# Optimization experiments

Hardware: AMD Instinct MI355X
Metric: run time of the kernel (lower is better)

The kernel has to match this reference:

```python
import jax, jax.numpy as jnp
import numpy as np
import math

B, S, E, H, NL, OUT, VOCAB = 16, 512, 1024, 16, 6, 10, 16
D = E // H
PAD = VOCAB - 1
EPS = 1e-5


def _positional_encoding():
    # Faithful to the module: pe[:x.size(0)] indexes the BATCH dim of a
    # [B, S, E] tensor, yielding [B, 1, E] broadcast over sequence.
    pos = jnp.arange(B, dtype=jnp.float32)[:, None]            # [B,1]
    div = jnp.exp(jnp.arange(0, E, 2, dtype=jnp.float32) * (-math.log(10000.0) / E))
    pe = jnp.zeros((B, E), dtype=jnp.float32)
    pe = pe.at[:, 0::2].set(jnp.sin(pos * div))
    pe = pe.at[:, 1::2].set(jnp.cos(pos * div))
    return pe[:, None, :]                                      # [B,1,E]


def setup_inputs() -> dict:
    key = jax.random.key(0)
    ks = jax.random.split(key, 8)
    sc = 0.02
    return {
        "inputs": jax.random.randint(ks[0], (B, S), 0, PAD),   # no pad tokens
        "emb": jax.random.normal(ks[1], (VOCAB, E), jnp.float32) * sc,
        "wq": jax.random.normal(ks[2], (E, E), jnp.float32) * sc,
        "bq": jnp.zeros((E,), jnp.float32),
        "wk": jax.random.normal(ks[3], (E, E), jnp.float32) * sc,
        "bk": jnp.zeros((E,), jnp.float32),
        "wv": jax.random.normal(ks[4], (E, E), jnp.float32) * sc,
        "bv": jnp.zeros((E,), jnp.float32),
        "wfc": jax.random.normal(ks[5], (E, E), jnp.float32) * sc,
        "bfc": jnp.zeros((E,), jnp.float32),
        "gamma": jnp.ones((E,), jnp.float32),
        "beta": jnp.zeros((E,), jnp.float32),
        "wout": jax.random.normal(ks[6], (S * E, OUT), jnp.float32) * sc,
        "bout": jnp.zeros((OUT,), jnp.float32),
    }


def _layernorm(x, gamma, beta):
    mu = jnp.mean(x, axis=-1, keepdims=True)
    var = jnp.mean(jnp.square(x - mu), axis=-1, keepdims=True)
    return (x - mu) * jax.lax.rsqrt(var + EPS) * gamma + beta


def reference(inputs, emb, wq, bq, wk, bk, wv, bv, wfc, bfc, gamma, beta, wout, bout):
    x = emb[inputs]                                            # [B,S,E]
    x = x + (x + _positional_encoding())                       # x += pos_enc(x)
    mask = (inputs == PAD)                                     # [B,S] key-pad mask
    scale = 1.0 / math.sqrt(D)
    for _ in range(NL):  # same (shared) weights each iteration, as in source
        q = (x @ wq + bq).reshape(B, S, H, D).transpose(0, 2, 1, 3)
        k = (x @ wk + bk).reshape(B, S, H, D).transpose(0, 2, 1, 3)
        v = (x @ wv + bv).reshape(B, S, H, D).transpose(0, 2, 1, 3)
        att = jnp.einsum('bhqd,bhkd->bhqk', q, k) * scale      # [B,H,S,S]
        att = jnp.where(mask[:, None, None, :], -jnp.inf, att)
        att = jax.nn.softmax(att, axis=-1)
        o = jnp.einsum('bhqk,bhkd->bhqd', att, v)
        o = o.transpose(0, 2, 1, 3).reshape(B, S, E)
        x = _layernorm(o + x, gamma, beta)                     # dropout = eval identity
        x = _layernorm((x @ wfc + bfc) + x, gamma, beta)
    return x.reshape(B, -1) @ wout + bout                      # [B,OUT]
```

## Files before the change

kernel.cpp:

```cpp
#include <hip/hip_runtime.h>
#include <hip/hip_bf16.h>
#include <math.h>

#define B_   16
#define S_   512
#define E_   1024
#define H_   16
#define D_   64
#define NL_  6
#define OUT_ 10
#define M_   (B_*S_)

typedef short short8 __attribute__((ext_vector_type(8)));
typedef float f32x4 __attribute__((ext_vector_type(4)));
typedef int   int4v __attribute__((ext_vector_type(4)));
typedef unsigned short ushort4v __attribute__((ext_vector_type(4)));

typedef const __attribute__((address_space(1))) unsigned int* gas1_t;
typedef __attribute__((address_space(3))) unsigned int* las3_t;
#define GLD16(g,l) __builtin_amdgcn_global_load_lds((gas1_t)(g), (las3_t)(l), 16, 0, 0)

static __device__ __forceinline__ float bf2f(unsigned short u){
  union { unsigned int i; float f; } v; v.i = ((unsigned int)u) << 16; return v.f;
}
static __device__ __forceinline__ unsigned short f2bf(float f){
  union { float f; unsigned int i; } v; v.f = f;
  unsigned int r = v.i + 0x7fffu + ((v.i >> 16) & 1u);
  return (unsigned short)(r >> 16);
}
static __device__ __forceinline__ f32x4 mfma16(short8 a, short8 b, f32x4 c){
  return __builtin_amdgcn_mfma_f32_16x16x32_bf16(a, b, c, 0, 0, 0);
}

__global__ __launch_bounds__(192)
void code_k(float* __restrict__ out, float code)
{
  int t = threadIdx.x;
  if (t < B_*OUT_) out[t] = code;
}

__global__ __launch_bounds__(256)
void transpose_k(const float* __restrict__ w0, const float* __restrict__ w1,
                 const float* __restrict__ w2, const float* __restrict__ w3,
                 unsigned short* __restrict__ wT)
{
  const float* w = blockIdx.z==0 ? w0 : blockIdx.z==1 ? w1 : blockIdx.z==2 ? w2 : w3;
  unsigned short* o = wT + (size_t)blockIdx.z * E_ * E_;
  __shared__ unsigned short tl[64][65];
  int n0 = blockIdx.x*64, k0 = blockIdx.y*64;
  int tx = threadIdx.x, ty = threadIdx.y;
  #pragma unroll
  for (int i = 0; i < 16; ++i)
    tl[ty + 4*i][tx] = f2bf(w[(size_t)(k0 + ty + 4*i)*E_ + n0 + tx]);
  __syncthreads();
  #pragma unroll
  for (int i = 0; i < 16; ++i)
    o[(size_t)(n0 + ty + 4*i)*E_ + k0 + tx] = tl[tx][ty + 4*i];
}

__global__ __launch_bounds__(256)
void embed_k(const int* __restrict__ tok, const float* __restrict__ emb,
             float* __restrict__ x, unsigned short* __restrict__ xb)
{
  int row = blockIdx.x;
  int b = row >> 9;
  int tk = tok[row];
  tk = tk < 0 ? 0 : (tk > 15 ? 15 : tk);
  int e0 = threadIdx.x * 4;
  const float c0 = -9.210340371976184f / (float)E_;
  f32x4 ev = *(const f32x4*)&emb[(size_t)tk * E_ + e0];
  f32x4 vv; ushort4v bb;
  #pragma unroll
  for (int i = 0; i < 4; ++i) {
    int e = e0 + i;
    float dv = expf((float)(e & ~1) * c0);
    float arg = (float)b * dv;
    float pe = (e & 1) ? cosf(arg) : sinf(arg);
    float v = 2.0f * ev[i] + pe;
    vv[i] = v; bb[i] = f2bf(v);
  }
  *(f32x4*)&x[(size_t)row*E_ + e0] = vv;
  *(ushort4v*)&xb[(size_t)row*E_ + e0] = bb;
}

template<int MODE>
__global__ __launch_bounds__(256)
void gemm_bt_k(const unsigned short* __restrict__ A,
               const unsigned short* __restrict__ BT,
               const float* __restrict__ biasA, const float* __restrict__ biasB,
               unsigned short* __restrict__ outq)
{
  __shared__ alignas(16) unsigned short SM[(MODE==2) ? 17408 : 16384];
  unsigned short* Al = SM;
  unsigned short* Bl = SM + 8192;
  int mt = blockIdx.x;
  int nyt = blockIdx.y;
  int wsel = (MODE == 0) ? (nyt >> 3) : 0;
  int nt   = (MODE == 0) ? (nyt & 7) : nyt;
  const unsigned short* Bp = BT + (size_t)wsel * E_ * E_ + (size_t)nt * 128 * E_;
  const float* bias = (MODE == 0) ? (wsel == 0 ? biasA : biasB) : biasA;
  int tid = threadIdx.x;
  int lane = tid & 63, wid = tid >> 6;
  int wr = wid >> 1, wc = wid & 1;
  int m0 = mt * 128;
  int lr = lane & 15, lk = lane >> 4;
  int lx = lr & 7;
  int c8 = tid & 7;
  int rbase = tid >> 3;
  int c8s = c8 ^ (rbase & 7);
  f32x4 acc[4][4] = {};
  for (int kt = 0; kt < E_/64; ++kt) {
    #pragma unroll
    for (int j = 0; j < 4; ++j) {
      int r = j*32 + rbase;
      int idx = j*256 + tid;
      GLD16(A + (size_t)(m0 + r)*E_ + kt*64 + c8s*8, &Al[idx*8]);
      GLD16(Bp + (size_t)r*E_ + kt*64 + c8s*8, &Bl[idx*8]);
    }
    __syncthreads();
    #pragma unroll
    for (int kk = 0; kk < 2; ++kk) {
      int sA = ((kk*4 + lk) ^ lx) * 8;
      short8 af[4], bfr[4];
      #pragma unroll
      for (int mi = 0; mi < 4; ++mi)
        af[mi] = *(const short8*)&Al[(wr*64 + mi*16 + lr)*64 + sA];
      #pragma unroll
      for (int ni = 0; ni < 4; ++ni)
        bfr[ni] = *(const short8*)&Bl[(wc*64 + ni*16 + lr)*64 + sA];
      #pragma unroll
      for (int mi = 0; mi < 4; ++mi)
        #pragma unroll
        for (int ni = 0; ni < 4; ++ni)
          acc[mi][ni] = mfma16(af[mi], bfr[ni], acc[mi][ni]);
    }
    __syncthreads();
  }
  if (MODE == 2) {
    unsigned short* Ct = SM;
    #pragma unroll
    for (int ni = 0; ni < 4; ++ni) {
      int nl = wc*64 + ni*16 + lr;
      float bv = bias[nt*128 + nl];
      #pragma unroll
      for (int mi = 0; mi < 4; ++mi)
        #pragma unroll
        for (int j = 0; j < 4; ++j)
          Ct[nl*136 + wr*64 + mi*16 + lk*4 + j] = f2bf(acc[mi][ni][j] + bv);
    }
    __syncthreads();
    int dl = tid >> 1, half = tid & 1;
    int h = nt*2 + (dl >> 6), d = dl & 63;
    int bb = m0 >> 9, s0 = (m0 & 511) + half*64;
    unsigned short* gp = outq + (((size_t)(bb*H_ + h)*D_ + d)*S_ + s0);
    #pragma unroll
    for (int c = 0; c < 8; ++c)
      *(int4v*)(gp + c*8) = *(const int4v*)&Ct[dl*136 + half*64 + c*8];
  } else {
    unsigned short* Cl = SM;
    #pragma unroll
    for (int ni = 0; ni < 4; ++ni) {
      int n = nt*128 + wc*64 + ni*16 + lr;
      float bv = bias[n];
      #pragma unroll
      for (int mi = 0; mi < 4; ++mi)
        #pragma unroll
        for (int j = 0; j < 4; ++j)
          Cl[(wr*64 + mi*16 + lk*4 + j)*128 + wc*64 + ni*16 + lr] =
            f2bf(acc[mi][ni][j] + bv);
    }
    __syncthreads();
    int r = tid >> 1, half = tid & 1;
    int m = m0 + r;
    unsigned short* gp;
    if (MODE == 0) {
      int bb = m >> 9, s = m & 511;
      int h = nt*2 + half;
      gp = outq + (size_t)wsel*M_*E_ + (((size_t)(bb*H_ + h)*S_ + s)*D_);
    } else {
      gp = outq + (size_t)m*E_ + nt*128 + half*64;
    }
    const unsigned short* sp = &Cl[r*128 + half*64];
    #pragma unroll
    for (int c = 0; c < 8; ++c)
      *(int4v*)(gp + c*8) = *(const int4v*)(sp + c*8);
  }
}

__global__ __launch_bounds__(512, 4)
void attn_k(const unsigned short* __restrict__ Q, const unsigned short* __restrict__ K,
            const unsigned short* __restrict__ VT, unsigned short* __restrict__ O)
{
  extern __shared__ unsigned short SMEM[];
  int bid = blockIdx.x;
  int bh = bid & 255, qh = bid >> 8;
  int tid = threadIdx.x, lane = tid & 63, wid = tid >> 6;
  int lr = lane & 15, lk = lane >> 4;
  const unsigned short* Qb = Q + (size_t)bh * S_ * D_;
  const unsigned short* Kb = K + (size_t)bh * S_ * D_;
  const unsigned short* VTb = VT + (size_t)bh * S_ * D_;
  unsigned short* Pw = SMEM + 32768 + wid * 640;

  int kr  = tid >> 3, kc8 = tid & 7;
  int kcs = kc8 ^ (kr & 7);
  int vd  = tid >> 4, vc16 = tid & 15;
  int vcs = vc16 ^ (vd & 15);

  short8 qf[2][2];
  #pragma unroll
  for (int s = 0; s < 2; ++s) {
    int q0 = (qh*2 + s)*128 + wid*16;
    qf[s][0] = *(const short8*)(Qb + (size_t)(q0 + lr)*D_ + lk*8);
    qf[s][1] = *(const short8*)(Qb + (size_t)(q0 + lr)*D_ + 32 + lk*8);
  }

  {
    unsigned short* Kd = SMEM;
    unsigned short* Vd = SMEM + 16384;
    #pragma unroll
    for (int j = 0; j < 2; ++j) {
      int idx = j*512 + tid;
      int r = (j*512 + tid) >> 3;
      (void)r;
      GLD16(Kb + (size_t)(kr + j*64)*D_ + kcs*8, &Kd[idx*8]);
      GLD16(VTb + (size_t)(vd)*S_ + (j*64 + 0)*0 + 0 + ((size_t)0) + (vcs*8) + ((size_t)(j)*0), &Vd[idx*8]);
    }
  }
  __syncthreads();

  {
    unsigned short* Vd = SMEM + 16384;
    #pragma unroll
    for (int j = 0; j < 2; ++j) {
      int idx = j*512 + tid;
      int d = idx >> 4, c16 = idx & 15;
      int cs = c16 ^ (d & 15);
      GLD16(VTb + (size_t)d*S_ + cs*8, &Vd[idx*8]);
    }
  }
  __syncthreads();

  f32x4 oacc[2][4] = {};
  float plsum[2][4] = {{0.f,0.f,0.f,0.f},{0.f,0.f,0.f,0.f}};
  int cur = 0;
  for (int kt = 0; kt < 4; ++kt) {
    if (kt < 3) {
      unsigned short* Kd = SMEM + (cur^1)*8192;
      unsigned short* Vd = SMEM + 16384 + (cur^1)*8192;
      #pragma unroll
      for (int j = 0; j < 2; ++j) {
        int idx = j*512 + tid;
        int r = idx >> 3, c8 = idx & 7;
        GLD16(Kb + (size_t)((kt+1)*128 + r)*D_ + (c8 ^ (r & 7))*8, &Kd[idx*8]);
        int d = idx >> 4, c16 = idx & 15;
        GLD16(VTb + (size_t)d*S_ + (kt+1)*128 + (c16 ^ (d & 15))*8, &Vd[idx*8]);
      }
    }
    const unsigned short* Kl = SMEM + cur*8192;
    const unsigned short* Vl = SMEM + 16384 + cur*8192;
    #pragma unroll
    for (int s = 0; s < 2; ++s) {
      #pragma unroll
      for (int c = 0; c < 4; ++c) {
        f32x4 s0 = {}, s1 = {};
        {
          const unsigned short* kr0 = &Kl[((2*c)*16 + lr)*64];
          const unsigned short* kr1 = &Kl[((2*c+1)*16 + lr)*64];
          int a0 = ((lk     ^ (lr & 7)))*8;
          int a1 = (((4+lk) ^ (lr & 7)))*8;
          s0 = mfma16(qf[s][0], *(const short8*)(kr0 + a0), s0);
          s0 = mfma16(qf[s][1], *(const short8*)(kr0 + a1), s0);
          s1 = mfma16(qf[s][0], *(const short8*)(kr1 + a0), s1);
          s1 = mfma16(qf[s][1], *(const short8*)(kr1 + a1), s1);
        }
        #pragma unroll
        for (int j = 0; j < 4; ++j) {
          s0[j] = __expf(s0[j] * 0.125f);
          s1[j] = __expf(s1[j] * 0.125f);
          plsum[s][j] += s0[j] + s1[j];
        }
        #pragma unroll
        for (int j = 0; j < 4; ++j) {
          Pw[(lk*4 + j)*40 + lr]      = f2bf(s0[j]);
          Pw[(lk*4 + j)*40 + 16 + lr] = f2bf(s1[j]);
        }
        asm volatile("s_waitcnt lgkmcnt(0)" ::: "memory");
        short8 pf = *(const short8*)&Pw[lr*40 + lk*8];
        #pragma unroll
        for (int dt = 0; dt < 4; ++dt) {
          int drow = dt*16 + lr;
          short8 vf = *(const short8*)&Vl[drow*128 + (((c*4 + lk) ^ lr))*8];
          oacc[s][dt] = mfma16(pf, vf, oacc[s][dt]);
        }
      }
    }
    __syncthreads();
    cur ^= 1;
  }
  #pragma unroll
  for (int s = 0; s < 2; ++s) {
    float lsum[4];
    #pragma unroll
    for (int j = 0; j < 4; ++j) {
      float t = plsum[s][j];
      #pragma unroll
      for (int m = 1; m < 16; m <<= 1) t += __shfl_xor(t, m);
      lsum[j] = t;
    }
    int q0 = (qh*2 + s)*128 + wid*16;
    #pragma unroll
    for (int dt = 0; dt < 4; ++dt)
      #pragma unroll
      for (int j = 0; j < 4; ++j)
        O[(size_t)bh*S_*D_ + (size_t)(q0 + lk*4 + j)*D_ + dt*16 + lr] =
          f2bf(oacc[s][dt][j] / lsum[j]);
  }
}

template<bool PERM>
__global__ __launch_bounds__(256)
void ln_k(const unsigned short* __restrict__ g, float* __restrict__ x,
          unsigned short* __restrict__ xb,
          const float* __restrict__ gamma, const float* __restrict__ beta)
{
  int row = blockIdx.x;
  int tid = threadIdx.x;
  int e0 = tid * 4;
  ushort4v gu;
  if (PERM) {
    int b = row >> 9, s = row & 511;
    int h = e0 >> 6, d = e0 & 63;
    gu = *(const ushort4v*)&g[(((size_t)(b*H_ + h)*S_) + s)*D_ + d];
  } else {
    gu = *(const ushort4v*)&g[(size_t)row*E_ + e0];
  }
  f32x4 xv = *(const f32x4*)&x[(size_t)row*E_ + e0];
  f32x4 v;
  #pragma unroll
  for (int i = 0; i < 4; ++i) v[i] = bf2f(gu[i]) + xv[i];
  float sum = v[0]+v[1]+v[2]+v[3];
  float sq  = v[0]*v[0]+v[1]*v[1]+v[2]*v[2]+v[3]*v[3];
  #pragma unroll
  for (int m = 1; m < 64; m <<= 1) { sum += __shfl_xor(sum, m); sq += __shfl_xor(sq, m); }
  __shared__ float red[2][4];
  int lane = tid & 63, wid = tid >> 6;
  if (lane == 0) { red[0][wid] = sum; red[1][wid] = sq; }
  __syncthreads();
  float ts = red[0][0]+red[0][1]+red[0][2]+red[0][3];
  float tq = red[1][0]+red[1][1]+red[1][2]+red[1][3];
  float mu = ts * (1.0f/E_);
  float var = tq * (1.0f/E_) - mu*mu;
  float rsq = rsqrtf(var + 1e-5f);
  f32x4 y; ushort4v yb;
  #pragma unroll
  for (int i = 0; i < 4; ++i) {
    float t = (v[i]-mu)*rsq*gamma[e0+i] + beta[e0+i];
    y[i] = t; yb[i] = f2bf(t);
  }
  *(f32x4*)&x[(size_t)row*E_ + e0] = y;
  *(ushort4v*)&xb[(size_t)row*E_ + e0] = yb;
}

__global__ __launch_bounds__(256)
void outp_k(const float* __restrict__ x, const float* __restrict__ wout,
            float* __restrict__ part)
{
  int b = blockIdx.y;
  int chunk = blockIdx.x;
  int tid = threadIdx.x;
  float acc[OUT_] = {};
  const float* xr = x + (size_t)b * S_ * E_;
  for (int j = 0; j < 32; ++j) {
    int k = chunk*8192 + j*256 + tid;
    float xv = xr[k];
    const float* wr = wout + (size_t)k * OUT_;
    #pragma unroll
    for (int o = 0; o < OUT_; ++o) acc[o] += xv * wr[o];
  }
  #pragma unroll
  for (int o = 0; o < OUT_; ++o)
    #pragma unroll
    for (int m = 1; m < 64; m <<= 1) acc[o] += __shfl_xor(acc[o], m);
  __shared__ float red[4][OUT_];
  int lane = tid & 63, wid = tid >> 6;
  if (lane == 0) {
    #pragma unroll
    for (int o = 0; o < OUT_; ++o) red[wid][o] = acc[o];
  }
  __syncthreads();
  if (tid < OUT_) {
    float s = red[0][tid] + red[1][tid] + red[2][tid] + red[3][tid];
    part[((size_t)chunk*B_ + b)*OUT_ + tid] = s;
  }
}

__global__ __launch_bounds__(192)
void outred_k(const float* __restrict__ part, const float* __restrict__ bout,
              float* __restrict__ out)
{
  int t = threadIdx.x;
  if (t < B_*OUT_) {
    int b = t / OUT_, o = t % OUT_;
    float s = 0.f;
    for (int c = 0; c < 64; ++c) s += part[((size_t)c*B_ + b)*OUT_ + o];
    s += bout[o];
    out[t] = s;
  }
}

extern "C" void kernel_launch(void* const* d_in, const int* in_sizes, int n_in,
                              void* d_out, int out_size, void* d_ws, size_t ws_size,
                              hipStream_t stream)
{
  (void)out_size;
  float* outb = (float*)d_out;

  static const int expect[14] = {8192, 16384, 1048576, 1024, 1048576, 1024,
                                 1048576, 1024, 1048576, 1024, 1024, 1024,
                                 5242880, 10};
  if (n_in != 14) { code_k<<<dim3(1), dim3(192), 0, stream>>>(outb, 9000.0f); return; }
  for (int i = 0; i < 14; ++i)
    if (in_sizes[i] != expect[i]) {
      code_k<<<dim3(1), dim3(192), 0, stream>>>(outb, 5000.0f + 100.0f*i); return;
    }

  const int* tok = (const int*)d_in[0];
  const float* emb  = (const float*)d_in[1];
  const float* wq   = (const float*)d_in[2];
  const float* bq   = (const float*)d_in[3];
  const float* wk   = (const float*)d_in[4];
  const float* bk   = (const float*)d_in[5];
  const float* wv   = (const float*)d_in[6];
  const float* bv   = (const float*)d_in[7];
  const float* wfc  = (const float*)d_in[8];
  const float* bfc  = (const float*)d_in[9];
  const float* gam  = (const float*)d_in[10];
  const float* bet  = (const float*)d_in[11];
  const float* wout = (const float*)d_in[12];
  const float* bout = (const float*)d_in[13];

  char* ws = (char*)d_ws;
  size_t off = 0;
  unsigned short* wT = (unsigned short*)(ws + off); off += (size_t)4*E_*E_*2;
  float* x  = (float*)(ws + off);                   off += (size_t)M_*E_*4;
  unsigned short* xb = (unsigned short*)(ws + off); off += (size_t)M_*E_*2;
  unsigned short* qkvb = (unsigned short*)(ws + off); off += (size_t)3*M_*E_*2;
  unsigned short* gb = (unsigned short*)(ws + off); off += (size_t)M_*E_*2;
  float* part = (float*)(ws + off);                 off += (size_t)64*B_*OUT_*4;
  if (off > ws_size) { code_k<<<dim3(1), dim3(192), 0, stream>>>(outb, 9500.0f); return; }

  transpose_k<<<dim3(16,16,4), dim3(64,4), 0, stream>>>(wq, wk, wv, wfc, wT);
  embed_k<<<dim3(M_), dim3(256), 0, stream>>>(tok, emb, x, xb);
  unsigned short* qb = qkvb;
  unsigned short* kb = qkvb + (size_t)M_*E_;
  unsigned short* vb = qkvb + (size_t)2*M_*E_;
  for (int l = 0; l < NL_; ++l) {
    gemm_bt_k<0><<<dim3(64,16), dim3(256), 0, stream>>>(xb, wT, bq, bk, qkvb);
    gemm_bt_k<2><<<dim3(64,8),  dim3(256), 0, stream>>>(xb, wT + (size_t)2*E_*E_, bv, bv, vb);
    attn_k<<<dim3(512), dim3(512), 75776, stream>>>(qb, kb, vb, gb);
    ln_k<true><<<dim3(M_), dim3(256), 0, stream>>>(gb, x, xb, gam, bet);
    gemm_bt_k<1><<<dim3(64,8), dim3(256), 0, stream>>>(xb, wT + (size_t)3*E_*E_, bfc, bfc, gb);
    ln_k<false><<<dim3(M_), dim3(256), 0, stream>>>(gb, x, xb, gam, bet);
  }
  outp_k<<<dim3(64,B_), dim3(256), 0, stream>>>(x, wout, part);
  outred_k<<<dim3(1), dim3(192), 0, stream>>>(part, bout, outb);
}
```

Before: 1.040 ms.

## Replace 128x128 GEMMs with double-buffered 256x256 GEMM and fuse QKV launches

Introduces a 512-thread GEMM kernel with 256x256 output tiles and double-buffered LDS. It issues global_load_lds prefetches for the next k-tile in four phases, each followed by explicit vmcnt waits and barriers, and raises wave priority around the MFMA section. Q, K and V projections now run in a single launch, with V transposed through LDS in the epilogue, while Q/K and the FC output use direct scattered bf16 stores. The attention kernel also drops a redundant initial V tile load and one barrier. The larger tiles cut redundant operand loads, but the grids shrink to 384 and 128 blocks with 128KB of LDS each, which risks idle CUs and wave imbalance, especially for the FC projection.

New measurement: 1.075 ms. 1.03x slower.

```diff
diff --git a/kernel.cpp b/kernel.cpp
--- a/kernel.cpp
+++ b/kernel.cpp
@@ -19,6 +19,7 @@
 typedef const __attribute__((address_space(1))) unsigned int* gas1_t;
 typedef __attribute__((address_space(3))) unsigned int* las3_t;
 #define GLD16(g,l) __builtin_amdgcn_global_load_lds((gas1_t)(g), (las3_t)(l), 16, 0, 0)
+#define VMW(n) asm volatile("s_waitcnt vmcnt(" #n ")" ::: "memory")
 
 static __device__ __forceinline__ float bf2f(unsigned short u){
   union { unsigned int i; float f; } v; v.i = ((unsigned int)u) << 16; return v.f;
@@ -84,106 +85,143 @@
 }
 
 template<int MODE>
-__global__ __launch_bounds__(256)
-void gemm_bt_k(const unsigned short* __restrict__ A,
-               const unsigned short* __restrict__ BT,
-               const float* __restrict__ biasA, const float* __restrict__ biasB,
-               unsigned short* __restrict__ outq)
-{
-  __shared__ alignas(16) unsigned short SM[(MODE==2) ? 17408 : 16384];
-  unsigned short* Al = SM;
-  unsigned short* Bl = SM + 8192;
-  int mt = blockIdx.x;
-  int nyt = blockIdx.y;
-  int wsel = (MODE == 0) ? (nyt >> 3) : 0;
-  int nt   = (MODE == 0) ? (nyt & 7) : nyt;
-  const unsigned short* Bp = BT + (size_t)wsel * E_ * E_ + (size_t)nt * 128 * E_;
-  const float* bias = (MODE == 0) ? (wsel == 0 ? biasA : biasB) : biasA;
-  int tid = threadIdx.x;
-  int lane = tid & 63, wid = tid >> 6;
-  int wr = wid >> 1, wc = wid & 1;
-  int m0 = mt * 128;
-  int lr = lane & 15, lk = lane >> 4;
-  int lx = lr & 7;
-  int c8 = tid & 7;
-  int rbase = tid >> 3;
-  int c8s = c8 ^ (rbase & 7);
-  f32x4 acc[4][4] = {};
-  for (int kt = 0; kt < E_/64; ++kt) {
-    #pragma unroll
-    for (int j = 0; j < 4; ++j) {
-      int r = j*32 + rbase;
-      int idx = j*256 + tid;
-      GLD16(A + (size_t)(m0 + r)*E_ + kt*64 + c8s*8, &Al[idx*8]);
-      GLD16(Bp + (size_t)r*E_ + kt*64 + c8s*8, &Bl[idx*8]);
+__global__ __launch_bounds__(512, 2)
+void gemm256_k(const unsigned short* __restrict__ A,
+               const unsigned short* __restrict__ WT,
+               const float* __restrict__ bq, const float* __restrict__ bk,
+               const float* __restrict__ bv,
+               unsigned short* __restrict__ out)
+{
+  extern __shared__ unsigned short SM2[];
+  int mt = blockIdx.x, nt = blockIdx.y;
+  int wsel = (MODE==0) ? (nt>>2) : 3;
+  int ntl  = (MODE==0) ? (nt&3)  : nt;
+  const unsigned short* Bp = WT + (MODE==0 ? (size_t)wsel*E_*E_ : (size_t)0) + (size_t)ntl*256*E_;
+  const float* bias = (MODE==0) ? (wsel==0 ? bq : (wsel==1 ? bk : bv)) : bq;
+  int m0 = mt*256;
+  int tid = threadIdx.x, lane = tid&63, wid = tid>>6;
+  int lr = lane&15, lk = lane>>4;
+  int rl = tid>>3;
+  int cs = (tid&7) ^ (rl&7);
+  unsigned short* Ab0 = SM2;
+  unsigned short* Ab1 = SM2 + 16384;
+  unsigned short* Bb0 = SM2 + 32768;
+  unsigned short* Bb1 = SM2 + 49152;
+
+  f32x4 acc[16][2] = {};
+
+  auto stA = [&](unsigned short* dst, int kt, int q) {
+    GLD16(A + (size_t)(m0 + q*64 + rl)*E_ + kt*64 + cs*8, dst + ((q*512 + tid)<<3));
+  };
+  auto stB = [&](unsigned short* dst, int kt, int h) {
+    GLD16(Bp + (size_t)(h*128 + rl)*E_ + kt*64 + cs*8,      dst + ((h*1024 + tid)<<3));
+    GLD16(Bp + (size_t)(h*128 + 64 + rl)*E_ + kt*64 + cs*8, dst + ((h*1024 + 512 + tid)<<3));
+  };
+
+  stB(Bb0, 0, 0); stB(Bb0, 0, 1);
+  stA(Ab0, 0, 0); stA(Ab0, 0, 1); stA(Ab0, 0, 2); stA(Ab0, 0, 3);
+
+  int sw0 = (lk ^ (lr&7)) << 3;
+  int sw1 = ((4+lk) ^ (lr&7)) << 3;
+  for (int kt = 0; kt < 16; ++kt) {
+    unsigned short* Ar = (kt & 1) ? Ab1 : Ab0;
+    unsigned short* Br = (kt & 1) ? Bb1 : Bb0;
+    unsigned short* An = (kt & 1) ? Ab0 : Ab1;
+    unsigned short* Bn = (kt & 1) ? Bb0 : Bb1;
+    bool more = (kt < 15);
+    #pragma unroll
+    for (int p = 0; p < 4; ++p) {
+      if (more) {
+        if (p == 0)      { stB(Bn, kt+1, 0); VMW(5); }
+        else if (p == 1) { stB(Bn, kt+1, 1); VMW(6); }
+        else if (p == 2) { stA(An, kt+1, 0); stA(An, kt+1, 1); VMW(7); }
+        else             { stA(An, kt+1, 2); stA(An, kt+1, 3); VMW(8); }
+      } else {
+        if (p == 0)      VMW(3);
+        else if (p == 1) VMW(2);
+        else if (p == 2) VMW(1);
+        else             VMW(0);
+      }
+      __builtin_amdgcn_s_barrier();
+      short8 af[4][2], bfr[2][2];
+      #pragma unroll
+      for (int i = 0; i < 4; ++i) {
+        int row = (p*4 + i)*16 + lr;
+        af[i][0] = *(const short8*)&Ar[row*64 + sw0];
+        af[i][1] = *(const short8*)&Ar[row*64 + sw1];
+      }
+      #pragma unroll
+      for (int ni = 0; ni < 2; ++ni) {
+        int row = wid*32 + ni*16 + lr;
+        bfr[ni][0] = *(const short8*)&Br[row*64 + sw0];
+        bfr[ni][1] = *(const short8*)&Br[row*64 + sw1];
+      }
+      __builtin_amdgcn_s_setprio(1);
+      #pragma unroll
+      for (int kk = 0; kk < 2; ++kk)
+        #pragma unroll
+        for (int i = 0; i < 4; ++i)
+          #pragma unroll
+          for (int ni = 0; ni < 2; ++ni)
+            acc[p*4+i][ni] = mfma16(af[i][kk], bfr[ni][kk], acc[p*4+i][ni]);
+      __builtin_amdgcn_s_setprio(0);
+      __builtin_amdgcn_s_barrier();
+    }
+  }
+
+  if (MODE == 1) {
+    #pragma unroll
+    for (int ni = 0; ni < 2; ++ni) {
+      int n = ntl*256 + wid*32 + ni*16 + lr;
+      float bv2 = bias[n];
+      #pragma unroll
+      for (int mi = 0; mi < 16; ++mi)
+        #pragma unroll
+        for (int j = 0; j < 4; ++j) {
+          int m = m0 + mi*16 + lk*4 + j;
+          out[(size_t)m*E_ + n] = f2bf(acc[mi][ni][j] + bv2);
+        }
+    }
+  } else if (wsel < 2) {
+    #pragma unroll
+    for (int ni = 0; ni < 2; ++ni) {
+      int n = ntl*256 + wid*32 + ni*16 + lr;
+      float bv2 = bias[n];
+      int h = n >> 6, d = n & 63;
+      #pragma unroll
+      for (int mi = 0; mi < 16; ++mi)
+        #pragma unroll
+        for (int j = 0; j < 4; ++j) {
+          int m = m0 + mi*16 + lk*4 + j;
+          int b = m >> 9, s = m & 511;
+          out[(size_t)wsel*M_*E_ + (((size_t)(b*H_ + h)*S_ + s)*D_ + d)] =
+            f2bf(acc[mi][ni][j] + bv2);
+        }
+    }
+  } else {
+    unsigned short* Cs = SM2;
+    #pragma unroll
+    for (int ni = 0; ni < 2; ++ni) {
+      int nl = wid*32 + ni*16 + lr;
+      float bv2 = bias[ntl*256 + nl];
+      #pragma unroll
+      for (int mi = 0; mi < 16; ++mi)
+        #pragma unroll
+        for (int j = 0; j < 4; ++j)
+          Cs[nl*256 + mi*16 + lk*4 + j] = f2bf(acc[mi][ni][j] + bv2);
     }
     __syncthreads();
-    #pragma unroll
-    for (int kk = 0; kk < 2; ++kk) {
-      int sA = ((kk*4 + lk) ^ lx) * 8;
-      short8 af[4], bfr[4];
-      #pragma unroll
-      for (int mi = 0; mi < 4; ++mi)
-        af[mi] = *(const short8*)&Al[(wr*64 + mi*16 + lr)*64 + sA];
-      #pragma unroll
-      for (int ni = 0; ni < 4; ++ni)
-        bfr[ni] = *(const short8*)&Bl[(wc*64 + ni*16 + lr)*64 + sA];
-      #pragma unroll
-      for (int mi = 0; mi < 4; ++mi)
-        #pragma unroll
-        for (int ni = 0; ni < 4; ++ni)
-          acc[mi][ni] = mfma16(af[mi], bfr[ni], acc[mi][ni]);
-    }
-    __syncthreads();
-  }
-  if (MODE == 2) {
-    unsigned short* Ct = SM;
-    #pragma unroll
-    for (int ni = 0; ni < 4; ++ni) {
-      int nl = wc*64 + ni*16 + lr;
-      float bv = bias[nt*128 + nl];
-      #pragma unroll
-      for (int mi = 0; mi < 4; ++mi)
-        #pragma unroll
-        for (int j = 0; j < 4; ++j)
-          Ct[nl*136 + wr*64 + mi*16 + lk*4 + j] = f2bf(acc[mi][ni][j] + bv);
-    }
-    __syncthreads();
-    int dl = tid >> 1, half = tid & 1;
-    int h = nt*2 + (dl >> 6), d = dl & 63;
-    int bb = m0 >> 9, s0 = (m0 & 511) + half*64;
-    unsigned short* gp = outq + (((size_t)(bb*H_ + h)*D_ + d)*S_ + s0);
-    #pragma unroll
-    for (int c = 0; c < 8; ++c)
-      *(int4v*)(gp + c*8) = *(const int4v*)&Ct[dl*136 + half*64 + c*8];
-  } else {
-    unsigned short* Cl = SM;
-    #pragma unroll
-    for (int ni = 0; ni < 4; ++ni) {
-      int n = nt*128 + wc*64 + ni*16 + lr;
-      float bv = bias[n];
-      #pragma unroll
-      for (int mi = 0; mi < 4; ++mi)
-        #pragma unroll
-        for (int j = 0; j < 4; ++j)
-          Cl[(wr*64 + mi*16 + lk*4 + j)*128 + wc*64 + ni*16 + lr] =
-            f2bf(acc[mi][ni][j] + bv);
-    }
-    __syncthreads();
-    int r = tid >> 1, half = tid & 1;
-    int m = m0 + r;
-    unsigned short* gp;
-    if (MODE == 0) {
-      int bb = m >> 9, s = m & 511;
-      int h = nt*2 + half;
-      gp = outq + (size_t)wsel*M_*E_ + (((size_t)(bb*H_ + h)*S_ + s)*D_);
-    } else {
-      gp = outq + (size_t)m*E_ + nt*128 + half*64;
-    }
-    const unsigned short* sp = &Cl[r*128 + half*64];
-    #pragma unroll
-    for (int c = 0; c < 8; ++c)
-      *(int4v*)(gp + c*8) = *(const int4v*)(sp + c*8);
+    int b = m0 >> 9, s0 = m0 & 511;
+    #pragma unroll
+    for (int j = 0; j < 16; ++j) {
+      int id = j*512 + tid;
+      int nl = id >> 5, mc = id & 31;
+      int n = ntl*256 + nl;
+      int h = n >> 6, d = n & 63;
+      unsigned short* gp = out + (size_t)2*M_*E_ +
+                           (((size_t)(b*H_ + h)*D_ + d)*S_ + s0 + mc*8);
+      *(int4v*)gp = *(const int4v*)&Cs[nl*256 + mc*8];
+    }
   }
 }
 
@@ -203,9 +241,6 @@
 
   int kr  = tid >> 3, kc8 = tid & 7;
   int kcs = kc8 ^ (kr & 7);
-  int vd  = tid >> 4, vc16 = tid & 15;
-  int vcs = vc16 ^ (vd & 15);
-
   short8 qf[2][2];
   #pragma unroll
   for (int s = 0; s < 2; ++s) {
@@ -213,29 +248,22 @@
     qf[s][0] = *(const short8*)(Qb + (size_t)(q0 + lr)*D_ + lk*8);
     qf[s][1] = *(const short8*)(Qb + (size_t)(q0 + lr)*D_ + 32 + lk*8);
   }
-
   {
     unsigned short* Kd = SMEM;
-    unsigned short* Vd = SMEM + 16384;
     #pragma unroll
     for (int j = 0; j < 2; ++j) {
       int idx = j*512 + tid;
-      int r = (j*512 + tid) >> 3;
-      (void)r;
       GLD16(Kb + (size_t)(kr + j*64)*D_ + kcs*8, &Kd[idx*8]);
-      GLD16(VTb + (size_t)(vd)*S_ + (j*64 + 0)*0 + 0 + ((size_t)0) + (vcs*8) + ((size_t)(j)*0), &Vd[idx*8]);
-    }
-  }
-  __syncthreads();
-
+    }
+  }
   {
     unsigned short* Vd = SMEM + 16384;
     #pragma unroll
     for (int j = 0; j < 2; ++j) {
       int idx = j*512 + tid;
       int d = idx >> 4, c16 = idx & 15;
-      int cs = c16 ^ (d & 15);
-      GLD16(VTb + (size_t)d*S_ + cs*8, &Vd[idx*8]);
+      int cds = c16 ^ (d & 15);
+      GLD16(VTb + (size_t)d*S_ + cds*8, &Vd[idx*8]);
     }
   }
   __syncthreads();
@@ -455,11 +483,10 @@
   unsigned short* kb = qkvb + (size_t)M_*E_;
   unsigned short* vb = qkvb + (size_t)2*M_*E_;
   for (int l = 0; l < NL_; ++l) {
-    gemm_bt_k<0><<<dim3(64,16), dim3(256), 0, stream>>>(xb, wT, bq, bk, qkvb);
-    gemm_bt_k<2><<<dim3(64,8),  dim3(256), 0, stream>>>(xb, wT + (size_t)2*E_*E_, bv, bv, vb);
+    gemm256_k<0><<<dim3(32,12), dim3(512), 131072, stream>>>(xb, wT, bq, bk, bv, qkvb);
     attn_k<<<dim3(512), dim3(512), 75776, stream>>>(qb, kb, vb, gb);
     ln_k<true><<<dim3(M_), dim3(256), 0, stream>>>(gb, x, xb, gam, bet);
-    gemm_bt_k<1><<<dim3(64,8), dim3(256), 0, stream>>>(xb, wT + (size_t)3*E_*E_, bfc, bfc, gb);
+    gemm256_k<1><<<dim3(32,4), dim3(512), 131072, stream>>>(xb, wT + (size_t)3*E_*E_, bfc, bfc, bfc, gb);
     ln_k<false><<<dim3(M_), dim3(256), 0, stream>>>(gb, x, xb, gam, bet);
   }
   outp_k<<<dim3(64,B_), dim3(256), 0, stream>>>(x, wout, part);
```

## Keep residual stream only in bf16 and drop redundant V prefetch in attention

Applied to the files above, without the earlier changes.

Removes the fp32 copy of the residual activations, so embedding, layernorm and the output projection read and write a single bf16 buffer. This cuts per-layer memory traffic in the layernorm kernels and the final projection. The attention kernel also drops a duplicated initial V tile load and one barrier. The trade is lower residual precision across six layers, which could shift accuracy.

After: 983.1 us. -5.5%, faster.

```diff
diff --git a/kernel.cpp b/kernel.cpp
--- a/kernel.cpp
+++ b/kernel.cpp
@@ -60,7 +60,7 @@
 
 __global__ __launch_bounds__(256)
 void embed_k(const int* __restrict__ tok, const float* __restrict__ emb,
-             float* __restrict__ x, unsigned short* __restrict__ xb)
+             unsigned short* __restrict__ x)
 {
   int row = blockIdx.x;
   int b = row >> 9;
@@ -69,18 +69,16 @@
   int e0 = threadIdx.x * 4;
   const float c0 = -9.210340371976184f / (float)E_;
   f32x4 ev = *(const f32x4*)&emb[(size_t)tk * E_ + e0];
-  f32x4 vv; ushort4v bb;
+  ushort4v bb;
   #pragma unroll
   for (int i = 0; i < 4; ++i) {
     int e = e0 + i;
     float dv = expf((float)(e & ~1) * c0);
     float arg = (float)b * dv;
     float pe = (e & 1) ? cosf(arg) : sinf(arg);
-    float v = 2.0f * ev[i] + pe;
-    vv[i] = v; bb[i] = f2bf(v);
-  }
-  *(f32x4*)&x[(size_t)row*E_ + e0] = vv;
-  *(ushort4v*)&xb[(size_t)row*E_ + e0] = bb;
+    bb[i] = f2bf(2.0f * ev[i] + pe);
+  }
+  *(ushort4v*)&x[(size_t)row*E_ + e0] = bb;
 }
 
 template<int MODE>
@@ -203,9 +201,6 @@
 
   int kr  = tid >> 3, kc8 = tid & 7;
   int kcs = kc8 ^ (kr & 7);
-  int vd  = tid >> 4, vc16 = tid & 15;
-  int vcs = vc16 ^ (vd & 15);
-
   short8 qf[2][2];
   #pragma unroll
   for (int s = 0; s < 2; ++s) {
@@ -213,29 +208,22 @@
     qf[s][0] = *(const short8*)(Qb + (size_t)(q0 + lr)*D_ + lk*8);
     qf[s][1] = *(const short8*)(Qb + (size_t)(q0 + lr)*D_ + 32 + lk*8);
   }
-
   {
     unsigned short* Kd = SMEM;
-    unsigned short* Vd = SMEM + 16384;
     #pragma unroll
     for (int j = 0; j < 2; ++j) {
       int idx = j*512 + tid;
-      int r = (j*512 + tid) >> 3;
-      (void)r;
       GLD16(Kb + (size_t)(kr + j*64)*D_ + kcs*8, &Kd[idx*8]);
-      GLD16(VTb + (size_t)(vd)*S_ + (j*64 + 0)*0 + 0 + ((size_t)0) + (vcs*8) + ((size_t)(j)*0), &Vd[idx*8]);
-    }
-  }
-  __syncthreads();
-
+    }
+  }
   {
     unsigned short* Vd = SMEM + 16384;
     #pragma unroll
     for (int j = 0; j < 2; ++j) {
       int idx = j*512 + tid;
       int d = idx >> 4, c16 = idx & 15;
-      int cs = c16 ^ (d & 15);
-      GLD16(VTb + (size_t)d*S_ + cs*8, &Vd[idx*8]);
+      int cds = c16 ^ (d & 15);
+      GLD16(VTb + (size_t)d*S_ + cds*8, &Vd[idx*8]);
     }
   }
   __syncthreads();
@@ -319,8 +307,7 @@
 
 template<bool PERM>
 __global__ __launch_bounds__(256)
-void ln_k(const unsigned short* __restrict__ g, float* __restrict__ x,
-          unsigned short* __restrict__ xb,
+void ln_k(const unsigned short* __restrict__ g, unsigned short* __restrict__ x,
           const float* __restrict__ gamma, const float* __restrict__ beta)
 {
   int row = blockIdx.x;
@@ -334,10 +321,10 @@
   } else {
     gu = *(const ushort4v*)&g[(size_t)row*E_ + e0];
   }
-  f32x4 xv = *(const f32x4*)&x[(size_t)row*E_ + e0];
+  ushort4v xu = *(const ushort4v*)&x[(size_t)row*E_ + e0];
   f32x4 v;
   #pragma unroll
-  for (int i = 0; i < 4; ++i) v[i] = bf2f(gu[i]) + xv[i];
+  for (int i = 0; i < 4; ++i) v[i] = bf2f(gu[i]) + bf2f(xu[i]);
   float sum = v[0]+v[1]+v[2]+v[3];
   float sq  = v[0]*v[0]+v[1]*v[1]+v[2]*v[2]+v[3]*v[3];
   #pragma unroll
@@ -351,28 +338,25 @@
   float mu = ts * (1.0f/E_);
   float var = tq * (1.0f/E_) - mu*mu;
   float rsq = rsqrtf(var + 1e-5f);
-  f32x4 y; ushort4v yb;
-  #pragma unroll
-  for (int i = 0; i < 4; ++i) {
-    float t = (v[i]-mu)*rsq*gamma[e0+i] + beta[e0+i];
-    y[i] = t; yb[i] = f2bf(t);
-  }
-  *(f32x4*)&x[(size_t)row*E_ + e0] = y;
-  *(ushort4v*)&xb[(size_t)row*E_ + e0] = yb;
+  ushort4v yb;
+  #pragma unroll
+  for (int i = 0; i < 4; ++i)
+    yb[i] = f2bf((v[i]-mu)*rsq*gamma[e0+i] + beta[e0+i]);
+  *(ushort4v*)&x[(size_t)row*E_ + e0] = yb;
 }
 
 __global__ __launch_bounds__(256)
-void outp_k(const float* __restrict__ x, const float* __restrict__ wout,
+void outp_k(const unsigned short* __restrict__ x, const float* __restrict__ wout,
             float* __restrict__ part)
 {
   int b = blockIdx.y;
   int chunk = blockIdx.x;
   int tid = threadIdx.x;
   float acc[OUT_] = {};
-  const float* xr = x + (size_t)b * S_ * E_;
+  const unsigned short* xr = x + (size_t)b * S_ * E_;
   for (int j = 0; j < 32; ++j) {
     int k = chunk*8192 + j*256 + tid;
-    float xv = xr[k];
+    float xv = bf2f(xr[k]);
     const float* wr = wout + (size_t)k * OUT_;
     #pragma unroll
     for (int o = 0; o < OUT_; ++o) acc[o] += xv * wr[o];
@@ -442,25 +426,24 @@
   char* ws = (char*)d_ws;
   size_t off = 0;
   unsigned short* wT = (unsigned short*)(ws + off); off += (size_t)4*E_*E_*2;
-  float* x  = (float*)(ws + off);                   off += (size_t)M_*E_*4;
-  unsigned short* xb = (unsigned short*)(ws + off); off += (size_t)M_*E_*2;
+  unsigned short* x  = (unsigned short*)(ws + off); off += (size_t)M_*E_*2;
   unsigned short* qkvb = (unsigned short*)(ws + off); off += (size_t)3*M_*E_*2;
   unsigned short* gb = (unsigned short*)(ws + off); off += (size_t)M_*E_*2;
   float* part = (float*)(ws + off);                 off += (size_t)64*B_*OUT_*4;
   if (off > ws_size) { code_k<<<dim3(1), dim3(192), 0, stream>>>(outb, 9500.0f); return; }
 
   transpose_k<<<dim3(16,16,4), dim3(64,4), 0, stream>>>(wq, wk, wv, wfc, wT);
-  embed_k<<<dim3(M_), dim3(256), 0, stream>>>(tok, emb, x, xb);
+  embed_k<<<dim3(M_), dim3(256), 0, stream>>>(tok, emb, x);
   unsigned short* qb = qkvb;
   unsigned short* kb = qkvb + (size_t)M_*E_;
   unsigned short* vb = qkvb + (size_t)2*M_*E_;
   for (int l = 0; l < NL_; ++l) {
-    gemm_bt_k<0><<<dim3(64,16), dim3(256), 0, stream>>>(xb, wT, bq, bk, qkvb);
-    gemm_bt_k<2><<<dim3(64,8),  dim3(256), 0, stream>>>(xb, wT + (size_t)2*E_*E_, bv, bv, vb);
+    gemm_bt_k<0><<<dim3(64,16), dim3(256), 0, stream>>>(x, wT, bq, bk, qkvb);
+    gemm_bt_k<2><<<dim3(64,8),  dim3(256), 0, stream>>>(x, wT + (size_t)2*E_*E_, bv, bv, vb);
     attn_k<<<dim3(512), dim3(512), 75776, stream>>>(qb, kb, vb, gb);
-    ln_k<true><<<dim3(M_), dim3(256), 0, stream>>>(gb, x, xb, gam, bet);
-    gemm_bt_k<1><<<dim3(64,8), dim3(256), 0, stream>>>(xb, wT + (size_t)3*E_*E_, bfc, bfc, gb);
-    ln_k<false><<<dim3(M_), dim3(256), 0, stream>>>(gb, x, xb, gam, bet);
+    ln_k<true><<<dim3(M_), dim3(256), 0, stream>>>(gb, x, gam, bet);
+    gemm_bt_k<1><<<dim3(64,8), dim3(256), 0, stream>>>(x, wT + (size_t)3*E_*E_, bfc, bfc, gb);
+    ln_k<false><<<dim3(M_), dim3(256), 0, stream>>>(gb, x, gam, bet);
   }
   outp_k<<<dim3(64,B_), dim3(256), 0, stream>>>(x, wout, part);
   outred_k<<<dim3(1), dim3(192), 0, stream>>>(part, bout, outb);
```
